# Kernel optimization log

Hardware: AMD Instinct MI355X
Metric: run time of the kernel (lower is better)

## Reference

```python
import jax, jax.numpy as jnp
import numpy as np

D_MODEL = 768
D_STATE = 16
D_CONV = 4
EXPAND = 2
D_INNER = EXPAND * D_MODEL          # 1536
DT_RANK = (D_MODEL + 15) // 16      # 48 (mamba default: ceil(d_model/16))


def setup_inputs() -> dict:
    key = jax.random.key(0)
    ks = jax.random.split(key, 8)
    B, T = 2, 1024
    s = 0.02
    return {
        "x": jax.random.normal(ks[0], (B, T, D_MODEL), jnp.float32),
        "ln_g": jnp.ones((D_MODEL,), jnp.float32),
        "ln_b": jnp.zeros((D_MODEL,), jnp.float32),
        "W_in": jax.random.normal(ks[1], (2 * D_INNER, D_MODEL), jnp.float32) * s,
        "conv_w": jax.random.normal(ks[2], (D_INNER, 1, D_CONV), jnp.float32) * s,
        "conv_b": jnp.zeros((D_INNER,), jnp.float32),
        "W_xproj": jax.random.normal(ks[3], (DT_RANK + 2 * D_STATE, D_INNER), jnp.float32) * s,
        "W_dt": jax.random.normal(ks[4], (D_INNER, DT_RANK), jnp.float32) * s,
        "b_dt": jax.random.normal(ks[5], (D_INNER,), jnp.float32) * s,
        "A_log": jnp.log(jnp.broadcast_to(jnp.arange(1.0, D_STATE + 1.0, dtype=jnp.float32), (D_INNER, D_STATE))),
        "Dp": jnp.ones((D_INNER,), jnp.float32),
        "W_out": jax.random.normal(ks[6], (D_MODEL, D_INNER), jnp.float32) * s,
    }


def _mamba_block(x, ln_g, ln_b, W_in, conv_w, conv_b, W_xproj, W_dt, b_dt, A_log, Dp, W_out):
    B, T, D = x.shape
    # LayerNorm
    mu = x.mean(-1, keepdims=True)
    var = ((x - mu) ** 2).mean(-1, keepdims=True)
    h = (x - mu) * jax.lax.rsqrt(var + 1e-5) * ln_g + ln_b
    # in_proj -> [B,T,2*d_inner], split into x-branch and gate z
    xz = h @ W_in.T
    xs, z = jnp.split(xz, 2, axis=-1)
    # causal depthwise conv over time (pad left d_conv-1), then SiLU
    xc = jax.lax.conv_general_dilated(
        xs.transpose(0, 2, 1), conv_w, (1,), [(D_CONV - 1, 0)],
        dimension_numbers=("NCH", "OIH", "NCH"), feature_group_count=D_INNER)
    xc = jax.nn.silu(xc.transpose(0, 2, 1) + conv_b)  # [B,T,d_inner]
    # x_proj -> dt_rank + 2*d_state
    x_dbl = xc @ W_xproj.T
    dt_r = x_dbl[..., :DT_RANK]
    Bm = x_dbl[..., DT_RANK:DT_RANK + D_STATE]       # [B,T,n]
    Cm = x_dbl[..., DT_RANK + D_STATE:]              # [B,T,n]
    dt = jax.nn.softplus(dt_r @ W_dt.T + b_dt)       # [B,T,d_inner]
    A = -jnp.exp(A_log)                              # [d_inner, n]
    dA = jnp.exp(jnp.einsum("btd,dn->btdn", dt, A))  # [B,T,d,n]
    dBu = jnp.einsum("btd,btn->btdn", dt * xc, Bm)   # [B,T,d,n]

    def step(s, inp):
        dA_t, dBu_t, C_t = inp
        s = dA_t * s + dBu_t                          # [B,d,n]
        y_t = jnp.einsum("bdn,bn->bd", s, C_t)
        return s, y_t

    s0 = jnp.zeros((B, D_INNER, D_STATE), x.dtype)
    _, ys = jax.lax.scan(step, s0,
                         (dA.transpose(1, 0, 2, 3), dBu.transpose(1, 0, 2, 3), Cm.transpose(1, 0, 2)))
    y = ys.transpose(1, 0, 2) + Dp * xc              # D skip connection
    y = y * jax.nn.silu(z)                           # gate
    return x + y @ W_out.T                           # out_proj + residual


def reference(x, ln_g, ln_b, W_in, conv_w, conv_b, W_xproj, W_dt, b_dt, A_log, Dp, W_out):
    return _mamba_block(x, ln_g, ln_b, W_in, conv_w, conv_b, W_xproj, W_dt, b_dt, A_log, Dp, W_out)
```

## Files before the change

### kernel.cpp

```cpp
#include <hip/hip_runtime.h>

typedef unsigned short u16;
typedef unsigned int u32;
typedef __attribute__((ext_vector_type(8))) short short8;
typedef __attribute__((ext_vector_type(8))) unsigned short ushort8;
typedef __attribute__((ext_vector_type(4))) float f32x4;

#define D_MODEL 768
#define D_INNER 1536
#define D_XZ    3072
#define D_STATE 16
#define DT_RANK 48
#define NROW    2048
#define SEQ     1024
#define XDS     128
#define NCHUNK  64
#define CLEN    16

typedef const __attribute__((address_space(1))) u32 glb_u32;
typedef __attribute__((address_space(3))) u32 lds_u32;

__device__ __forceinline__ float bf2f(u16 u) {
    union { unsigned int i; float f; } v; v.i = ((unsigned int)u) << 16; return v.f;
}
__device__ __forceinline__ u16 f2bf(float f) {
    union { float f; unsigned int i; } v; v.f = f;
    unsigned int r = v.i + 0x7fffu + ((v.i >> 16) & 1u);
    return (u16)(r >> 16);
}
__device__ __forceinline__ void g2lds16(const u16* g, u16* l) {
    __builtin_amdgcn_global_load_lds((glb_u32*)g, (lds_u32*)l, 16, 0, 0);
}

#define N0 (D_XZ * D_MODEL / 4)
#define N1 (D_MODEL * D_INNER / 4)
#define N2 (XDS * D_INNER / 4)
#define N3 (D_INNER * 64 / 4)
#define N4 (D_INNER * D_STATE / 4)
#define N5 (NROW * XDS / 4)
#define PREP_BLOCKS ((N0+N1+N2+N3+N4+N5) / 256)
__global__ __launch_bounds__(256) void prep_ln_k(
    const float* __restrict__ x, const float* __restrict__ g,
    const float* __restrict__ bln, u16* __restrict__ h,
    const float* __restrict__ W_in, const float* __restrict__ W_out,
    const float* __restrict__ W_xp, const float* __restrict__ W_dt,
    const float* __restrict__ A_log,
    u16* __restrict__ Win_bf, u16* __restrict__ Wout_bf,
    u16* __restrict__ Wxp_bf, u16* __restrict__ Wdt_bf,
    float* __restrict__ negA, float* __restrict__ xdbl)
{
    __shared__ float sred[4], sqred[4];
    int tid = threadIdx.x;
    if (blockIdx.x < NROW) {
        int row = blockIdx.x;
        const float* xr = x + (size_t)row * D_MODEL;
        float v[3], s = 0.f, sq = 0.f;
#pragma unroll
        for (int j = 0; j < 3; ++j) {
            v[j] = xr[tid + j * 256];
            s += v[j]; sq += v[j] * v[j];
        }
#pragma unroll
        for (int off = 32; off >= 1; off >>= 1) {
            s  += __shfl_xor(s,  off, 64);
            sq += __shfl_xor(sq, off, 64);
        }
        if ((tid & 63) == 0) { sred[tid >> 6] = s; sqred[tid >> 6] = sq; }
        __syncthreads();
        float st = sred[0] + sred[1] + sred[2] + sred[3];
        float sqt = sqred[0] + sqred[1] + sqred[2] + sqred[3];
        float mu = st * (1.f / D_MODEL);
        float var = sqt * (1.f / D_MODEL) - mu * mu;
        float rstd = rsqrtf(var + 1e-5f);
        u16* hr = h + (size_t)row * D_MODEL;
#pragma unroll
        for (int j = 0; j < 3; ++j) {
            int idx = tid + j * 256;
            hr[idx] = f2bf((v[j] - mu) * rstd * g[idx] + bln[idx]);
        }
        return;
    }
    int gid = (blockIdx.x - NROW) * 256 + tid;
    if (gid < N0) {
        float4 v = *(const float4*)(W_in + (size_t)gid * 4);
        u16* o = Win_bf + (size_t)gid * 4;
        o[0]=f2bf(v.x); o[1]=f2bf(v.y); o[2]=f2bf(v.z); o[3]=f2bf(v.w);
    } else if (gid < N0 + N1) {
        int i = gid - N0;
        float4 v = *(const float4*)(W_out + (size_t)i * 4);
        u16* o = Wout_bf + (size_t)i * 4;
        o[0]=f2bf(v.x); o[1]=f2bf(v.y); o[2]=f2bf(v.z); o[3]=f2bf(v.w);
    } else if (gid < N0 + N1 + N2) {
        int i = gid - N0 - N1;
        int n = (i * 4) / D_INNER, k = (i * 4) % D_INNER;
        u16* o = Wxp_bf + (size_t)i * 4;
        if (n < 80) {
            float4 v = *(const float4*)(W_xp + (size_t)n * D_INNER + k);
            o[0]=f2bf(v.x); o[1]=f2bf(v.y); o[2]=f2bf(v.z); o[3]=f2bf(v.w);
        } else { o[0]=0; o[1]=0; o[2]=0; o[3]=0; }
    } else if (gid < N0 + N1 + N2 + N3) {
        int i = gid - N0 - N1 - N2;
        int r = (i * 4) >> 6, c0 = (i * 4) & 63;
        u16* o = Wdt_bf + (size_t)i * 4;
        if (c0 < DT_RANK) {
            float4 v = *(const float4*)(W_dt + (size_t)r * DT_RANK + c0);
            o[0]=f2bf(v.x); o[1]=f2bf(v.y); o[2]=f2bf(v.z); o[3]=f2bf(v.w);
        } else { o[0]=0; o[1]=0; o[2]=0; o[3]=0; }
    } else if (gid < N0 + N1 + N2 + N3 + N4) {
        int i = gid - N0 - N1 - N2 - N3;
        float4 v = *(const float4*)(A_log + (size_t)i * 4);
        *(float4*)(negA + (size_t)i * 4) =
            make_float4(-__expf(v.x), -__expf(v.y), -__expf(v.z), -__expf(v.w));
    } else if (gid < N0 + N1 + N2 + N3 + N4 + N5) {
        int i = gid - N0 - N1 - N2 - N3 - N4;
        *(float4*)(xdbl + (size_t)i * 4) = make_float4(0.f, 0.f, 0.f, 0.f);
    }
}

template<int MT, int NT, bool OUT_BF16, bool ADD_RES>
__global__ __launch_bounds__(256) void gemm128(
    const u16* __restrict__ A, const u16* __restrict__ B,
    const float* __restrict__ Res, void* __restrict__ Cv,
    int M, int N, int K)
{
    constexpr int BM = 32 * MT, BN = 32 * NT;
    __shared__ __align__(16) u16 As[BM * 64];
    __shared__ __align__(16) u16 Bs[BN * 64];
    int tid = threadIdx.x, w = tid >> 6, lane = tid & 63;
    int wm = w & 1, wn = w >> 1;
    int m0 = blockIdx.x * BM, n0 = blockIdx.y * BN;
    int mloc = lane & 15, quad = lane >> 4;
    int lr8 = lane >> 3, lc8 = lane & 7;
    f32x4 acc[MT][NT] = {};

    for (int k0 = 0; k0 < K; k0 += 64) {
        __syncthreads();
#pragma unroll
        for (int j = w; j < BM / 8; j += 4) {
            int row = j * 8 + lr8;
            int cg = lc8 ^ (row & 7);
            g2lds16(A + (size_t)(m0 + row) * K + k0 + cg * 8, &As[j * 512]);
        }
#pragma unroll
        for (int j = w; j < BN / 8; j += 4) {
            int row = j * 8 + lr8;
            int cg = lc8 ^ (row & 7);
            g2lds16(B + (size_t)(n0 + row) * K + k0 + cg * 8, &Bs[j * 512]);
        }
        __syncthreads();
        short8 afr[MT][2], bfr[NT][2];
#pragma unroll
        for (int mt = 0; mt < MT; ++mt) {
            int row = wm * MT * 16 + mt * 16 + mloc;
#pragma unroll
            for (int h = 0; h < 2; ++h) {
                int pc = (h * 4 + quad) ^ (row & 7);
                afr[mt][h] = *(const short8*)(&As[row * 64 + pc * 8]);
            }
        }
#pragma unroll
        for (int nt = 0; nt < NT; ++nt) {
            int row = wn * NT * 16 + nt * 16 + mloc;
#pragma unroll
            for (int h = 0; h < 2; ++h) {
                int pc = (h * 4 + quad) ^ (row & 7);
                bfr[nt][h] = *(const short8*)(&Bs[row * 64 + pc * 8]);
            }
        }
#pragma unroll
        for (int h = 0; h < 2; ++h)
#pragma unroll
            for (int mt = 0; mt < MT; ++mt)
#pragma unroll
                for (int nt = 0; nt < NT; ++nt)
                    acc[mt][nt] = __builtin_amdgcn_mfma_f32_16x16x32_bf16(
                        afr[mt][h], bfr[nt][h], acc[mt][nt], 0, 0, 0);
    }
#pragma unroll
    for (int mt = 0; mt < MT; ++mt) {
        int grow0 = m0 + wm * MT * 16 + mt * 16 + quad * 4;
#pragma unroll
        for (int nt = 0; nt < NT; ++nt) {
            int gcol = n0 + wn * NT * 16 + nt * 16 + mloc;
#pragma unroll
            for (int r = 0; r < 4; ++r) {
                size_t idx = (size_t)(grow0 + r) * N + gcol;
                float v = acc[mt][nt][r];
                if (ADD_RES) v += Res[idx];
                if (OUT_BF16) ((u16*)Cv)[idx] = f2bf(v);
                else          ((float*)Cv)[idx] = v;
            }
        }
    }
}

template<int MT, int NT, int KSLICE>
__global__ __launch_bounds__(256) void gemm_splitk(
    const u16* __restrict__ A, const u16* __restrict__ B,
    float* __restrict__ Cout, int K, int CS)
{
    constexpr int BM = 32 * MT, BN = 32 * NT;
    __shared__ __align__(16) u16 As[BM * 64];
    __shared__ __align__(16) u16 Bs[BN * 64];
    int tid = threadIdx.x, w = tid >> 6, lane = tid & 63;
    int wm = w & 1, wn = w >> 1;
    int m0 = blockIdx.x * BM, n0 = blockIdx.y * BN;
    int kbase = blockIdx.z * KSLICE;
    int mloc = lane & 15, quad = lane >> 4;
    int lr8 = lane >> 3, lc8 = lane & 7;
    f32x4 acc[MT][NT] = {};

    for (int k0 = 0; k0 < KSLICE; k0 += 64) {
        __syncthreads();
#pragma unroll
        for (int j = w; j < BM / 8; j += 4) {
            int row = j * 8 + lr8;
            int cg = lc8 ^ (row & 7);
            g2lds16(A + (size_t)(m0 + row) * K + kbase + k0 + cg * 8, &As[j * 512]);
        }
#pragma unroll
        for (int j = w; j < BN / 8; j += 4) {
            int row = j * 8 + lr8;
            int cg = lc8 ^ (row & 7);
            g2lds16(B + (size_t)(n0 + row) * K + kbase + k0 + cg * 8, &Bs[j * 512]);
        }
        __syncthreads();
        short8 afr[MT][2], bfr[NT][2];
#pragma unroll
        for (int mt = 0; mt < MT; ++mt) {
            int row = wm * MT * 16 + mt * 16 + mloc;
#pragma unroll
            for (int h = 0; h < 2; ++h) {
                int pc = (h * 4 + quad) ^ (row & 7);
                afr[mt][h] = *(const short8*)(&As[row * 64 + pc * 8]);
            }
        }
#pragma unroll
        for (int nt = 0; nt < NT; ++nt) {
            int row = wn * NT * 16 + nt * 16 + mloc;
#pragma unroll
            for (int h = 0; h < 2; ++h) {
                int pc = (h * 4 + quad) ^ (row & 7);
                bfr[nt][h] = *(const short8*)(&Bs[row * 64 + pc * 8]);
            }
        }
#pragma unroll
        for (int h = 0; h < 2; ++h)
#pragma unroll
            for (int mt = 0; mt < MT; ++mt)
#pragma unroll
                for (int nt = 0; nt < NT; ++nt)
                    acc[mt][nt] = __builtin_amdgcn_mfma_f32_16x16x32_bf16(
                        afr[mt][h], bfr[nt][h], acc[mt][nt], 0, 0, 0);
    }
#pragma unroll
    for (int mt = 0; mt < MT; ++mt) {
        int grow0 = m0 + wm * MT * 16 + mt * 16 + quad * 4;
#pragma unroll
        for (int nt = 0; nt < NT; ++nt) {
            int gcol = n0 + wn * NT * 16 + nt * 16 + mloc;
#pragma unroll
            for (int r = 0; r < 4; ++r)
                unsafeAtomicAdd(&Cout[(size_t)(grow0 + r) * CS + gcol],
                                acc[mt][nt][r]);
        }
    }
}

__global__ __launch_bounds__(256) void dtgemm_k(
    const float* __restrict__ xdbl, const u16* __restrict__ Wdt,
    const float* __restrict__ bias, u16* __restrict__ dtout)
{
    __shared__ __align__(16) u16 Bs[64 * 72];
    int tid = threadIdx.x, wave = tid >> 6, lane = tid & 63;
    int m0 = blockIdx.x * 64, n0 = blockIdx.y * 64;
    int mloc = lane & 15, quad = lane >> 4;
    {
        int r = tid >> 3, ck = (tid & 7) * 8;
#pragma unroll
        for (int rr = 0; rr < 64; rr += 32) {
            int4 bv = *(const int4*)(Wdt + (size_t)(n0 + r + rr) * 64 + ck);
            *(int4*)(&Bs[(r + rr) * 72 + ck]) = bv;
        }
    }
    int arow = m0 + wave * 16 + mloc;
    const float* ar = xdbl + (size_t)arow * XDS + quad * 8;
    short8 af[2];
#pragma unroll
    for (int h = 0; h < 2; ++h) {
        float4 a0 = *(const float4*)(ar + h * 32);
        float4 a1 = *(const float4*)(ar + h * 32 + 4);
        short8 t;
        t[0]=(short)f2bf(a0.x); t[1]=(short)f2bf(a0.y);
        t[2]=(short)f2bf(a0.z); t[3]=(short)f2bf(a0.w);
        t[4]=(short)f2bf(a1.x); t[5]=(short)f2bf(a1.y);
        t[6]=(short)f2bf(a1.z); t[7]=(short)f2bf(a1.w);
        af[h] = t;
    }
    __syncthreads();
    f32x4 acc[4] = {};
#pragma unroll
    for (int h = 0; h < 2; ++h)
#pragma unroll
        for (int nt = 0; nt < 4; ++nt) {
            short8 bf = *(const short8*)(&Bs[(nt * 16 + mloc) * 72 + h * 32 + quad * 8]);
            acc[nt] = __builtin_amdgcn_mfma_f32_16x16x32_bf16(af[h], bf, acc[nt], 0, 0, 0);
        }
#pragma unroll
    for (int nt = 0; nt < 4; ++nt) {
        int gcol = n0 + nt * 16 + mloc;
        int grow = m0 + wave * 16 + quad * 4;
#pragma unroll
        for (int r = 0; r < 4; ++r) {
            float t = acc[nt][r] + bias[gcol];
            float sp = (t > 15.f) ? t : __logf(1.f + __expf(t));
            dtout[(size_t)(grow + r) * D_INNER + gcol] = f2bf(sp);
        }
    }
}

__global__ __launch_bounds__(256) void conv_silu_k(
    const u16* __restrict__ xz, const float* __restrict__ cw,
    const float* __restrict__ cb, u16* __restrict__ xc)
{
    int gid = blockIdx.x * 256 + threadIdx.x;
    int r = gid / (D_INNER / 4);
    int c4 = (gid - r * (D_INNER / 4)) * 4;
    int t = r & (SEQ - 1);
    float4 cbv = *(const float4*)(cb + c4);
    float acc[4] = {cbv.x, cbv.y, cbv.z, cbv.w};
    float4 wv[4];
#pragma unroll
    for (int j = 0; j < 4; ++j) wv[j] = *(const float4*)(cw + (c4 + j) * 4);
#pragma unroll
    for (int k = 0; k < 4; ++k) {
        int tt = t - 3 + k;
        if (tt >= 0) {
            ushort4 xv = *(const ushort4*)(xz + (size_t)(r - 3 + k) * D_XZ + c4);
            acc[0] += bf2f(xv.x) * ((const float*)&wv[0])[k];
            acc[1] += bf2f(xv.y) * ((const float*)&wv[1])[k];
            acc[2] += bf2f(xv.z) * ((const float*)&wv[2])[k];
            acc[3] += bf2f(xv.w) * ((const float*)&wv[3])[k];
        }
    }
    ushort4 o;
    o.x = f2bf(acc[0] / (1.f + __expf(-acc[0])));
    o.y = f2bf(acc[1] / (1.f + __expf(-acc[1])));
    o.z = f2bf(acc[2] / (1.f + __expf(-acc[2])));
    o.w = f2bf(acc[3] / (1.f + __expf(-acc[3])));
    *(ushort4*)(xc + (size_t)r * D_INNER + c4) = o;
}

__global__ __launch_bounds__(256) void scan_p1(
    const u16* __restrict__ dt, const u16* __restrict__ xc,
    const float* __restrict__ xdbl, const float* __restrict__ negA,
    u16* __restrict__ Sbuf, float* __restrict__ dtsumbuf)
{
    __shared__ float Bsh[CLEN][D_STATE];
    int tid = threadIdx.x;
    int gid = blockIdx.x * 256 + tid;
    int d = gid % D_INNER;
    int bcN = gid / D_INNER;
    int c = bcN % NCHUNK, b = bcN / NCHUNK;
    size_t r0 = (size_t)b * SEQ + c * CLEN;
    {
        int tt = tid >> 4, n = tid & 15;
        Bsh[tt][n] = xdbl[(r0 + tt) * XDS + DT_RANK + n];
    }
    float a[D_STATE], s[D_STATE] = {};
    {
        const float4* Ar = (const float4*)(negA + d * D_STATE);
        float4 a0 = Ar[0], a1 = Ar[1], a2 = Ar[2], a3 = Ar[3];
        a[0]=a0.x; a[1]=a0.y; a[2]=a0.z; a[3]=a0.w;
        a[4]=a1.x; a[5]=a1.y; a[6]=a1.z; a[7]=a1.w;
        a[8]=a2.x; a[9]=a2.y; a[10]=a2.z; a[11]=a2.w;
        a[12]=a3.x; a[13]=a3.y; a[14]=a3.z; a[15]=a3.w;
    }
    float dtv[CLEN], du[CLEN];
    const u16* dp = dt + r0 * D_INNER + d;
    const u16* xp = xc + r0 * D_INNER + d;
#pragma unroll
    for (int t = 0; t < CLEN; ++t) {
        dtv[t] = bf2f(dp[t * D_INNER]);
        du[t] = dtv[t] * bf2f(xp[t * D_INNER]);
    }
    __syncthreads();
    float dtsum = 0.f;
#pragma unroll
    for (int t = 0; t < CLEN; ++t) {
        dtsum += dtv[t];
#pragma unroll
        for (int n = 0; n < D_STATE; ++n)
            s[n] = __expf(dtv[t] * a[n]) * s[n] + du[t] * Bsh[t][n];
    }
    ushort8 so[2];
#pragma unroll
    for (int j = 0; j < 16; ++j) so[j >> 3][j & 7] = f2bf(s[j]);
    *(ushort8*)(Sbuf + (size_t)gid * D_STATE) = so[0];
    *(ushort8*)(Sbuf + (size_t)gid * D_STATE + 8) = so[1];
    dtsumbuf[gid] = dtsum;
}

__global__ __launch_bounds__(256) void scan_p2(
    const u16* __restrict__ Sbuf, const float* __restrict__ dtsumbuf,
    const float* __restrict__ negA, u16* __restrict__ carry)
{
    int gid = blockIdx.x * 256 + threadIdx.x;
    int n = gid % D_STATE;
    int d = (gid / D_STATE) % D_INNER;
    int b = gid / (D_STATE * D_INNER);
    float a = negA[d * D_STATE + n];
    float s = 0.f;
#pragma unroll 8
    for (int c = 0; c < NCHUNK; ++c) {
        size_t idx = ((size_t)(b * NCHUNK + c) * D_INNER + d);
        carry[idx * D_STATE + n] = f2bf(s);
        s = bf2f(Sbuf[idx * D_STATE + n]) + __expf(a * dtsumbuf[idx]) * s;
    }
}

__global__ __launch_bounds__(256) void scan_p3(
    const u16* __restrict__ dt, const u16* __restrict__ xc,
    const u16* __restrict__ xz, const float* __restrict__ xdbl,
    const float* __restrict__ negA, const float* __restrict__ Dp,
    const u16* __restrict__ carry, u16* __restrict__ yy)
{
    __shared__ float BCsh[CLEN][2 * D_STATE];
    int tid = threadIdx.x;
    int gid = blockIdx.x * 256 + tid;
    int d = gid % D_INNER;
    int bcN = gid / D_INNER;
    int c = bcN % NCHUNK, b = bcN / NCHUNK;
    size_t r0 = (size_t)b * SEQ + c * CLEN;
#pragma unroll
    for (int j = 0; j < 2; ++j) {
        int idx = tid + j * 256;
        int row = idx >> 5, col = idx & 31;
        BCsh[row][col] = xdbl[(r0 + row) * XDS + DT_RANK + col];
    }
    float a[D_STATE], s[D_STATE];
    {
        ushort8 c0 = *(const ushort8*)(carry + (size_t)gid * D_STATE);
        ushort8 c1 = *(const ushort8*)(carry + (size_t)gid * D_STATE + 8);
#pragma unroll
        for (int j = 0; j < 8; ++j) { s[j] = bf2f(c0[j]); s[8 + j] = bf2f(c1[j]); }
        const float4* Ar = (const float4*)(negA + d * D_STATE);
        float4 a0 = Ar[0], a1 = Ar[1], a2 = Ar[2], a3 = Ar[3];
        a[0]=a0.x; a[1]=a0.y; a[2]=a0.z; a[3]=a0.w;
        a[4]=a1.x; a[5]=a1.y; a[6]=a1.z; a[7]=a1.w;
        a[8]=a2.x; a[9]=a2.y; a[10]=a2.z; a[11]=a2.w;
        a[12]=a3.x; a[13]=a3.y; a[14]=a3.z; a[15]=a3.w;
    }
    float dtv[CLEN], xcv[CLEN], zv[CLEN];
    const u16* dp = dt + r0 * D_INNER + d;
    const u16* xp = xc + r0 * D_INNER + d;
    const u16* zp = xz + r0 * D_XZ + D_INNER + d;
#pragma unroll
    for (int t = 0; t < CLEN; ++t) {
        dtv[t] = bf2f(dp[t * D_INNER]);
        xcv[t] = bf2f(xp[t * D_INNER]);
        zv[t]  = bf2f(zp[t * D_XZ]);
    }
    float dpv = Dp[d];
    __syncthreads();
    u16* yp = yy + r0 * D_INNER + d;
#pragma unroll
    for (int t = 0; t < CLEN; ++t) {
        float du = dtv[t] * xcv[t];
        float y = 0.f;
#pragma unroll
        for (int n = 0; n < D_STATE; ++n) {
            s[n] = __expf(dtv[t] * a[n]) * s[n] + du * BCsh[t][n];
            y += s[n] * BCsh[t][D_STATE + n];
        }
        float yv = y + dpv * xcv[t];
        float sig = 1.f / (1.f + __expf(-zv[t]));
        yp[t * D_INNER] = f2bf(yv * (zv[t] * sig));
    }
}

extern "C" void kernel_launch(void* const* d_in, const int* in_sizes, int n_in,
                              void* d_out, int out_size, void* d_ws, size_t ws_size,
                              hipStream_t stream) {
    const float* x      = (const float*)d_in[0];
    const float* ln_g   = (const float*)d_in[1];
    const float* ln_b   = (const float*)d_in[2];
    const float* W_in   = (const float*)d_in[3];
    const float* conv_w = (const float*)d_in[4];
    const float* conv_b = (const float*)d_in[5];
    const float* W_xp   = (const float*)d_in[6];
    const float* W_dt   = (const float*)d_in[7];
    const float* b_dt   = (const float*)d_in[8];
    const float* A_log  = (const float*)d_in[9];
    const float* Dp     = (const float*)d_in[10];
    const float* W_out  = (const float*)d_in[11];
    float* out = (float*)d_out;

    char* ws = (char*)d_ws;
    u16*   h_bf    = (u16*)ws;   ws += (size_t)NROW * D_MODEL * 2;
    u16*   xz_bf   = (u16*)ws;   ws += (size_t)NROW * D_XZ * 2;
    u16*   xc_bf   = (u16*)ws;   ws += (size_t)NROW * D_INNER * 2;
    float* xdbl    = (float*)ws; ws += (size_t)NROW * XDS * 4;
    u16*   dtbuf   = (u16*)ws;   ws += (size_t)NROW * D_INNER * 2;
    u16*   yybuf   = (u16*)ws;   ws += (size_t)NROW * D_INNER * 2;
    u16*   Win_bf  = (u16*)ws;   ws += (size_t)D_XZ * D_MODEL * 2;
    u16*   Wout_bf = (u16*)ws;   ws += (size_t)D_MODEL * D_INNER * 2;
    u16*   Wxp_bf  = (u16*)ws;   ws += (size_t)XDS * D_INNER * 2;
    u16*   Wdt_bf  = (u16*)ws;   ws += (size_t)D_INNER * 64 * 2;
    float* negA    = (float*)ws; ws += (size_t)D_INNER * D_STATE * 4;
    u16*   Sbuf    = (u16*)ws;   ws += (size_t)2 * NCHUNK * D_INNER * 16 * 2;
    float* dtsumb  = (float*)ws; ws += (size_t)2 * NCHUNK * D_INNER * 4;
    u16*   carryb  = (u16*)ws;

    prep_ln_k<<<NROW + PREP_BLOCKS, 256, 0, stream>>>(
        x, ln_g, ln_b, h_bf, W_in, W_out, W_xp, W_dt, A_log,
        Win_bf, Wout_bf, Wxp_bf, Wdt_bf, negA, xdbl);

    gemm128<4, 2, true, false><<<dim3(NROW / 128, D_XZ / 64), 256, 0, stream>>>(
        h_bf, Win_bf, nullptr, xz_bf, NROW, D_XZ, D_MODEL);
    conv_silu_k<<<NROW * (D_INNER / 4) / 256, 256, 0, stream>>>(
        xz_bf, conv_w, conv_b, xc_bf);
    gemm_splitk<2, 4, 192><<<dim3(NROW / 64, 1, 8), 256, 0, stream>>>(
        xc_bf, Wxp_bf, xdbl, D_INNER, XDS);
    dtgemm_k<<<dim3(NROW / 64, D_INNER / 64), 256, 0, stream>>>(
        xdbl, Wdt_bf, b_dt, dtbuf);

    scan_p1<<<2 * NCHUNK * D_INNER / 256, 256, 0, stream>>>(
        dtbuf, xc_bf, xdbl, negA, Sbuf, dtsumb);
    scan_p2<<<2 * D_INNER * D_STATE / 256, 256, 0, stream>>>(
        Sbuf, dtsumb, negA, carryb);
    scan_p3<<<2 * NCHUNK * D_INNER / 256, 256, 0, stream>>>(
        dtbuf, xc_bf, xz_bf, xdbl, negA, Dp, carryb, yybuf);

    gemm128<2, 2, false, true><<<dim3(NROW / 64, D_MODEL / 64), 256, 0, stream>>>(
        yybuf, Wout_bf, x, out, NROW, D_MODEL, D_INNER);
}
```

Before: 185.1 us.

## Fuse dt projection with scan phase 1, split-K out_proj, batch conv rows

Merges the dt projection GEMM and the first chunked-scan pass into one kernel, so dt stays in shared memory for the per-chunk state computation and one launch plus a dt re-read go away. The causal conv now has each thread produce four consecutive time steps from a shared 7-row window, which cuts redundant loads. The output projection becomes a 2-way split-K atomic GEMM into an output buffer that the prep kernel pre-fills with the residual x. The risks are atomic float accumulation order in the output and a different chunk-to-block mapping in the scan pass.

After: 180.9 us. 2.3% less time.

```diff
diff --git a/kernel.cpp b/kernel.cpp
--- a/kernel.cpp
+++ b/kernel.cpp
@@ -38,7 +38,8 @@
 #define N3 (D_INNER * 64 / 4)
 #define N4 (D_INNER * D_STATE / 4)
 #define N5 (NROW * XDS / 4)
-#define PREP_BLOCKS ((N0+N1+N2+N3+N4+N5) / 256)
+#define N6 (NROW * D_MODEL / 4)
+#define PREP_BLOCKS ((N0+N1+N2+N3+N4+N5+N6) / 256)
 __global__ __launch_bounds__(256) void prep_ln_k(
     const float* __restrict__ x, const float* __restrict__ g,
     const float* __restrict__ bln, u16* __restrict__ h,
@@ -47,7 +48,8 @@
     const float* __restrict__ A_log,
     u16* __restrict__ Win_bf, u16* __restrict__ Wout_bf,
     u16* __restrict__ Wxp_bf, u16* __restrict__ Wdt_bf,
-    float* __restrict__ negA, float* __restrict__ xdbl)
+    float* __restrict__ negA, float* __restrict__ xdbl,
+    float* __restrict__ outres)
 {
     __shared__ float sred[4], sqred[4];
     int tid = threadIdx.x;
@@ -114,6 +116,9 @@
     } else if (gid < N0 + N1 + N2 + N3 + N4 + N5) {
         int i = gid - N0 - N1 - N2 - N3 - N4;
         *(float4*)(xdbl + (size_t)i * 4) = make_float4(0.f, 0.f, 0.f, 0.f);
+    } else if (gid < N0 + N1 + N2 + N3 + N4 + N5 + N6) {
+        int i = gid - N0 - N1 - N2 - N3 - N4 - N5;
+        *(float4*)(outres + (size_t)i * 4) = *(const float4*)(x + (size_t)i * 4);
     }
 }
 
@@ -267,11 +272,16 @@
     }
 }
 
-__global__ __launch_bounds__(256) void dtgemm_k(
+__global__ __launch_bounds__(256) void dtscan_k(
     const float* __restrict__ xdbl, const u16* __restrict__ Wdt,
-    const float* __restrict__ bias, u16* __restrict__ dtout)
+    const float* __restrict__ bias, const u16* __restrict__ xc,
+    const float* __restrict__ negA,
+    u16* __restrict__ dtout, u16* __restrict__ Sbuf,
+    float* __restrict__ dtsumbuf)
 {
     __shared__ __align__(16) u16 Bs[64 * 72];
+    __shared__ float Bsh[64][D_STATE];
+    __shared__ u16 dt_sh[64][68];
     int tid = threadIdx.x, wave = tid >> 6, lane = tid & 63;
     int m0 = blockIdx.x * 64, n0 = blockIdx.y * 64;
     int mloc = lane & 15, quad = lane >> 4;
@@ -283,90 +293,51 @@
             *(int4*)(&Bs[(r + rr) * 72 + ck]) = bv;
         }
     }
+    {
+        int row = tid >> 2, nn = (tid & 3) * 4;
+        *(float4*)(&Bsh[row][nn]) =
+            *(const float4*)(xdbl + (size_t)(m0 + row) * XDS + DT_RANK + nn);
+    }
     int arow = m0 + wave * 16 + mloc;
     const float* ar = xdbl + (size_t)arow * XDS + quad * 8;
     short8 af[2];
 #pragma unroll
-    for (int h = 0; h < 2; ++h) {
-        float4 a0 = *(const float4*)(ar + h * 32);
-        float4 a1 = *(const float4*)(ar + h * 32 + 4);
+    for (int hh = 0; hh < 2; ++hh) {
+        float4 a0 = *(const float4*)(ar + hh * 32);
+        float4 a1 = *(const float4*)(ar + hh * 32 + 4);
         short8 t;
         t[0]=(short)f2bf(a0.x); t[1]=(short)f2bf(a0.y);
         t[2]=(short)f2bf(a0.z); t[3]=(short)f2bf(a0.w);
         t[4]=(short)f2bf(a1.x); t[5]=(short)f2bf(a1.y);
         t[6]=(short)f2bf(a1.z); t[7]=(short)f2bf(a1.w);
-        af[h] = t;
+        af[hh] = t;
     }
     __syncthreads();
     f32x4 acc[4] = {};
 #pragma unroll
-    for (int h = 0; h < 2; ++h)
+    for (int hh = 0; hh < 2; ++hh)
 #pragma unroll
         for (int nt = 0; nt < 4; ++nt) {
-            short8 bf = *(const short8*)(&Bs[(nt * 16 + mloc) * 72 + h * 32 + quad * 8]);
-            acc[nt] = __builtin_amdgcn_mfma_f32_16x16x32_bf16(af[h], bf, acc[nt], 0, 0, 0);
+            short8 bf = *(const short8*)(&Bs[(nt * 16 + mloc) * 72 + hh * 32 + quad * 8]);
+            acc[nt] = __builtin_amdgcn_mfma_f32_16x16x32_bf16(af[hh], bf, acc[nt], 0, 0, 0);
         }
 #pragma unroll
     for (int nt = 0; nt < 4; ++nt) {
-        int gcol = n0 + nt * 16 + mloc;
-        int grow = m0 + wave * 16 + quad * 4;
+        int lcol = nt * 16 + mloc;
+        float bv = bias[n0 + lcol];
 #pragma unroll
         for (int r = 0; r < 4; ++r) {
-            float t = acc[nt][r] + bias[gcol];
+            int lrow = wave * 16 + quad * 4 + r;
+            float t = acc[nt][r] + bv;
             float sp = (t > 15.f) ? t : __logf(1.f + __expf(t));
-            dtout[(size_t)(grow + r) * D_INNER + gcol] = f2bf(sp);
-        }
-    }
-}
-
-__global__ __launch_bounds__(256) void conv_silu_k(
-    const u16* __restrict__ xz, const float* __restrict__ cw,
-    const float* __restrict__ cb, u16* __restrict__ xc)
-{
-    int gid = blockIdx.x * 256 + threadIdx.x;
-    int r = gid / (D_INNER / 4);
-    int c4 = (gid - r * (D_INNER / 4)) * 4;
-    int t = r & (SEQ - 1);
-    float4 cbv = *(const float4*)(cb + c4);
-    float acc[4] = {cbv.x, cbv.y, cbv.z, cbv.w};
-    float4 wv[4];
-#pragma unroll
-    for (int j = 0; j < 4; ++j) wv[j] = *(const float4*)(cw + (c4 + j) * 4);
-#pragma unroll
-    for (int k = 0; k < 4; ++k) {
-        int tt = t - 3 + k;
-        if (tt >= 0) {
-            ushort4 xv = *(const ushort4*)(xz + (size_t)(r - 3 + k) * D_XZ + c4);
-            acc[0] += bf2f(xv.x) * ((const float*)&wv[0])[k];
-            acc[1] += bf2f(xv.y) * ((const float*)&wv[1])[k];
-            acc[2] += bf2f(xv.z) * ((const float*)&wv[2])[k];
-            acc[3] += bf2f(xv.w) * ((const float*)&wv[3])[k];
-        }
-    }
-    ushort4 o;
-    o.x = f2bf(acc[0] / (1.f + __expf(-acc[0])));
-    o.y = f2bf(acc[1] / (1.f + __expf(-acc[1])));
-    o.z = f2bf(acc[2] / (1.f + __expf(-acc[2])));
-    o.w = f2bf(acc[3] / (1.f + __expf(-acc[3])));
-    *(ushort4*)(xc + (size_t)r * D_INNER + c4) = o;
-}
-
-__global__ __launch_bounds__(256) void scan_p1(
-    const u16* __restrict__ dt, const u16* __restrict__ xc,
-    const float* __restrict__ xdbl, const float* __restrict__ negA,
-    u16* __restrict__ Sbuf, float* __restrict__ dtsumbuf)
-{
-    __shared__ float Bsh[CLEN][D_STATE];
-    int tid = threadIdx.x;
-    int gid = blockIdx.x * 256 + tid;
-    int d = gid % D_INNER;
-    int bcN = gid / D_INNER;
-    int c = bcN % NCHUNK, b = bcN / NCHUNK;
-    size_t r0 = (size_t)b * SEQ + c * CLEN;
-    {
-        int tt = tid >> 4, n = tid & 15;
-        Bsh[tt][n] = xdbl[(r0 + tt) * XDS + DT_RANK + n];
-    }
+            u16 v = f2bf(sp);
+            dtout[(size_t)(m0 + lrow) * D_INNER + n0 + lcol] = v;
+            dt_sh[lrow][lcol] = v;
+        }
+    }
+    __syncthreads();
+    int d_loc = lane, c_loc = wave;
+    int d = n0 + d_loc;
     float a[D_STATE], s[D_STATE] = {};
     {
         const float4* Ar = (const float4*)(negA + d * D_STATE);
@@ -377,28 +348,69 @@
         a[12]=a3.x; a[13]=a3.y; a[14]=a3.z; a[15]=a3.w;
     }
     float dtv[CLEN], du[CLEN];
-    const u16* dp = dt + r0 * D_INNER + d;
-    const u16* xp = xc + r0 * D_INNER + d;
+    const u16* xp = xc + (size_t)(m0 + c_loc * CLEN) * D_INNER + d;
 #pragma unroll
     for (int t = 0; t < CLEN; ++t) {
-        dtv[t] = bf2f(dp[t * D_INNER]);
+        dtv[t] = bf2f(dt_sh[c_loc * CLEN + t][d_loc]);
         du[t] = dtv[t] * bf2f(xp[t * D_INNER]);
     }
-    __syncthreads();
     float dtsum = 0.f;
 #pragma unroll
     for (int t = 0; t < CLEN; ++t) {
         dtsum += dtv[t];
 #pragma unroll
         for (int n = 0; n < D_STATE; ++n)
-            s[n] = __expf(dtv[t] * a[n]) * s[n] + du[t] * Bsh[t][n];
-    }
+            s[n] = __expf(dtv[t] * a[n]) * s[n] + du[t] * Bsh[c_loc * CLEN + t][n];
+    }
+    size_t sidx = (size_t)(m0 / CLEN + c_loc) * D_INNER + d;
     ushort8 so[2];
 #pragma unroll
     for (int j = 0; j < 16; ++j) so[j >> 3][j & 7] = f2bf(s[j]);
-    *(ushort8*)(Sbuf + (size_t)gid * D_STATE) = so[0];
-    *(ushort8*)(Sbuf + (size_t)gid * D_STATE + 8) = so[1];
-    dtsumbuf[gid] = dtsum;
+    *(ushort8*)(Sbuf + sidx * D_STATE) = so[0];
+    *(ushort8*)(Sbuf + sidx * D_STATE + 8) = so[1];
+    dtsumbuf[sidx] = dtsum;
+}
+
+__global__ __launch_bounds__(256) void conv_silu_k(
+    const u16* __restrict__ xz, const float* __restrict__ cw,
+    const float* __restrict__ cb, u16* __restrict__ xc)
+{
+    int gid = blockIdx.x * 256 + threadIdx.x;
+    int rg = gid / (D_INNER / 4);
+    int c4 = (gid - rg * (D_INNER / 4)) * 4;
+    int r0 = rg * 4;
+    int t0 = r0 & (SEQ - 1);
+    float4 cbv = *(const float4*)(cb + c4);
+    float4 wv[4];
+#pragma unroll
+    for (int j = 0; j < 4; ++j) wv[j] = *(const float4*)(cw + (c4 + j) * 4);
+    float win[7][4];
+#pragma unroll
+    for (int j = 0; j < 7; ++j) {
+        if (j < 3 && t0 == 0) {
+            win[j][0] = 0.f; win[j][1] = 0.f; win[j][2] = 0.f; win[j][3] = 0.f;
+        } else {
+            ushort4 xv = *(const ushort4*)(xz + (size_t)(r0 - 3 + j) * D_XZ + c4);
+            win[j][0] = bf2f(xv.x); win[j][1] = bf2f(xv.y);
+            win[j][2] = bf2f(xv.z); win[j][3] = bf2f(xv.w);
+        }
+    }
+#pragma unroll
+    for (int i = 0; i < 4; ++i) {
+        float acc[4] = {cbv.x, cbv.y, cbv.z, cbv.w};
+#pragma unroll
+        for (int k = 0; k < 4; ++k) {
+#pragma unroll
+            for (int ch = 0; ch < 4; ++ch)
+                acc[ch] += win[i + k][ch] * ((const float*)&wv[ch])[k];
+        }
+        ushort4 o;
+        o.x = f2bf(acc[0] / (1.f + __expf(-acc[0])));
+        o.y = f2bf(acc[1] / (1.f + __expf(-acc[1])));
+        o.z = f2bf(acc[2] / (1.f + __expf(-acc[2])));
+        o.w = f2bf(acc[3] / (1.f + __expf(-acc[3])));
+        *(ushort4*)(xc + (size_t)(r0 + i) * D_INNER + c4) = o;
+    }
 }
 
 __global__ __launch_bounds__(256) void scan_p2(
@@ -514,24 +526,22 @@
 
     prep_ln_k<<<NROW + PREP_BLOCKS, 256, 0, stream>>>(
         x, ln_g, ln_b, h_bf, W_in, W_out, W_xp, W_dt, A_log,
-        Win_bf, Wout_bf, Wxp_bf, Wdt_bf, negA, xdbl);
+        Win_bf, Wout_bf, Wxp_bf, Wdt_bf, negA, xdbl, out);
 
     gemm128<4, 2, true, false><<<dim3(NROW / 128, D_XZ / 64), 256, 0, stream>>>(
         h_bf, Win_bf, nullptr, xz_bf, NROW, D_XZ, D_MODEL);
-    conv_silu_k<<<NROW * (D_INNER / 4) / 256, 256, 0, stream>>>(
+    conv_silu_k<<<(NROW / 4) * (D_INNER / 4) / 256, 256, 0, stream>>>(
         xz_bf, conv_w, conv_b, xc_bf);
     gemm_splitk<2, 4, 192><<<dim3(NROW / 64, 1, 8), 256, 0, stream>>>(
         xc_bf, Wxp_bf, xdbl, D_INNER, XDS);
-    dtgemm_k<<<dim3(NROW / 64, D_INNER / 64), 256, 0, stream>>>(
-        xdbl, Wdt_bf, b_dt, dtbuf);
-
-    scan_p1<<<2 * NCHUNK * D_INNER / 256, 256, 0, stream>>>(
-        dtbuf, xc_bf, xdbl, negA, Sbuf, dtsumb);
+    dtscan_k<<<dim3(NROW / 64, D_INNER / 64), 256, 0, stream>>>(
+        xdbl, Wdt_bf, b_dt, xc_bf, negA, dtbuf, Sbuf, dtsumb);
+
     scan_p2<<<2 * D_INNER * D_STATE / 256, 256, 0, stream>>>(
         Sbuf, dtsumb, negA, carryb);
     scan_p3<<<2 * NCHUNK * D_INNER / 256, 256, 0, stream>>>(
         dtbuf, xc_bf, xz_bf, xdbl, negA, Dp, carryb, yybuf);
 
-    gemm128<2, 2, false, true><<<dim3(NROW / 64, D_MODEL / 64), 256, 0, stream>>>(
-        yybuf, Wout_bf, x, out, NROW, D_MODEL, D_INNER);
-}
+    gemm_splitk<2, 2, 768><<<dim3(NROW / 64, D_MODEL / 64, 2), 256, 0, stream>>>(
+        yybuf, Wout_bf, out, D_INNER, D_MODEL);
+}
```
